# Performance work log

Measured on AMD Instinct MI355X. Metric: run time of the kernel, lower is better.

The kernel has to match this reference:

```python
import jax, jax.numpy as jnp
import numpy as np


def setup_inputs() -> dict:
    key = jax.random.key(0)
    ks = jax.random.split(key, 12)
    Tq, Tk, B, H = 1024, 1024, 8, 1024
    inp = {
        "inputs_q": jax.random.normal(ks[0], (Tq, B, H), jnp.float32),
        "inputs_kv": jax.random.normal(ks[1], (Tk, B, H), jnp.float32),
        "w_q": jax.random.normal(ks[2], (H, H), jnp.float32) * 0.02,
        "b_q": jnp.zeros((H,), jnp.float32),
        "w_kv": jax.random.normal(ks[3], (2 * H, H), jnp.float32) * 0.02,
        "b_kv": jnp.zeros((2 * H,), jnp.float32),
        "w_o": jax.random.normal(ks[4], (H, H), jnp.float32) * 0.02,
        "b_o": jnp.zeros((H,), jnp.float32),
        # BatchEnsemble rank-1 factors, initialized near 1
        "r_q": 1.0 + 0.05 * jax.random.normal(ks[5], (B, H), jnp.float32),
        "s_q": 1.0 + 0.05 * jax.random.normal(ks[6], (B, H), jnp.float32),
        "r_kv": 1.0 + 0.05 * jax.random.normal(ks[7], (B, H), jnp.float32),
        "s_kv": 1.0 + 0.05 * jax.random.normal(ks[8], (B, 2 * H), jnp.float32),
        "heads": 16,
    }
    return inp


def be_linear(x, w, b, r, s):
    # x: [T,B,Hin], w: [Hout,Hin], r: [B,Hin], s: [B,Hout]
    return jnp.einsum('tbh,oh->tbo', x * r, w) * s + b


def reference(inputs_q, inputs_kv, w_q, b_q, w_kv, b_kv, w_o, b_o,
              r_q, s_q, r_kv, s_kv, heads):
    Tq, B, H = inputs_q.shape
    Tk = inputs_kv.shape[0]
    hd = H // heads
    scale = hd ** -0.5

    q = be_linear(inputs_q, w_q, b_q, r_q, s_q)          # [Tq,B,H]
    kv = be_linear(inputs_kv, w_kv, b_kv, r_kv, s_kv)    # [Tk,B,2H]

    queries = q.reshape(Tq, B * heads, hd)
    kv = kv.reshape(Tk, B * heads, 2, hd)                # layout: head x {k,v} x hd
    keys = kv[:, :, 0, :]
    values = kv[:, :, 1, :]

    scores = jnp.einsum('qnd,knd->nqk', queries, keys) * scale  # [B*heads,Tq,Tk]
    probs = jax.nn.softmax(scores.astype(jnp.float32), axis=-1).astype(scores.dtype)
    # dropout_prob = 0 / eval: dropout is identity
    ctx = jnp.einsum('nqk,knd->qnd', probs, values).reshape(Tq, B, H)
    out = jnp.einsum('tbh,oh->tbo', ctx, w_o) + b_o      # [Tq,B,H]
    return out
```

## Files before the change

kernel.cpp:

```cpp
#include <hip/hip_runtime.h>
#include <stdint.h>

typedef unsigned short u16;
typedef __bf16 bf16x8 __attribute__((ext_vector_type(8)));
typedef float f32x4 __attribute__((ext_vector_type(4)));

typedef __attribute__((address_space(3))) void lds_void;
typedef const __attribute__((address_space(1))) void gbl_void;
#define GLD_LDS16(g, l) __builtin_amdgcn_global_load_lds((gbl_void*)(g), (lds_void*)(l), 16, 0, 0)

#define BAR_RELAX() asm volatile("s_waitcnt vmcnt(4)\n\ts_barrier" ::: "memory")
#define BAR_FULL()  asm volatile("s_waitcnt vmcnt(0)\n\ts_barrier" ::: "memory")

__device__ __forceinline__ u16 f2bf(float f) {
  unsigned u = __float_as_uint(f);
  u += 0x7fffu + ((u >> 16) & 1u);
  return (u16)(u >> 16);
}

__device__ __forceinline__ unsigned pk2bf(float a, float b) {
  unsigned au = __float_as_uint(a) + 0x8000u;
  unsigned bu = __float_as_uint(b) + 0x8000u;
  return __builtin_amdgcn_perm(bu, au, 0x07060302u);
}

__global__ void k_convert_all(const float* __restrict__ inq, const float* __restrict__ r_q,
                              const float* __restrict__ inkv, const float* __restrict__ r_kv,
                              const float* __restrict__ w_q, const float* __restrict__ w_kv,
                              const float* __restrict__ w_o,
                              u16* __restrict__ Xq, u16* __restrict__ Xkv,
                              u16* __restrict__ Wq, u16* __restrict__ Wkv,
                              u16* __restrict__ Wo) {
  int blk = blockIdx.x;
  const float* src; const float* r = nullptr; u16* dst; int base;
  if (blk < 8192)       { src = inq;  r = r_q;  dst = Xq;  base = 0; }
  else if (blk < 16384) { src = inkv; r = r_kv; dst = Xkv; base = 8192; }
  else if (blk < 17408) { src = w_q;  dst = Wq;  base = 16384; }
  else if (blk < 19456) { src = w_kv; dst = Wkv; base = 17408; }
  else                  { src = w_o;  dst = Wo;  base = 19456; }
  int i4 = ((blk - base) * 256 + threadIdx.x) * 4;
  float4 xv = *(const float4*)(src + i4);
  if (r) {
    int rb = ((i4 >> 10) & 7) * 1024 + (i4 & 1023);
    float4 rv = *(const float4*)(r + rb);
    xv.x *= rv.x; xv.y *= rv.y; xv.z *= rv.z; xv.w *= rv.w;
  }
  unsigned long long pk = (unsigned long long)pk2bf(xv.x, xv.y)
      | ((unsigned long long)pk2bf(xv.z, xv.w) << 32);
  *(unsigned long long*)(dst + i4) = pk;
}

template <int MODE>
__device__ __forceinline__ void gemm_tile(const u16* __restrict__ A, const u16* __restrict__ B,
                                          void* __restrict__ Cout, const float* __restrict__ s,
                                          const float* __restrict__ bias, int N, int K,
                                          float postscale, int bx, int by,
                                          u16* As, u16* Bs, int tid,
                                          u16* __restrict__ vt, int h) {
  const int w = tid >> 6, lane = tid & 63;
  const int quad = lane >> 4, l16 = lane & 15;
  const int n0 = bx * 128, m0 = by * 128;
  const int wm = (w & 1) * 64, wn = (w >> 1) * 64;

  f32x4 acc[4][4] = {};

  int srow[2], scol[2];
#pragma unroll
  for (int i = 0; i < 2; ++i) {
    int p = (w * 2 + i) * 64 + lane;
    int row = p >> 2;
    int cb = (p & 3) ^ ((row >> 1) & 3);
    srow[i] = row; scol[i] = cb * 8;
  }
  int offA[4], offB[4];
#pragma unroll
  for (int t = 0; t < 4; ++t) {
    int ra = wm + t * 16 + l16;
    offA[t] = ra * 32 + ((quad ^ ((ra >> 1) & 3)) * 8);
    int rb = wn + t * 16 + l16;
    offB[t] = rb * 32 + ((quad ^ ((rb >> 1) & 3)) * 8);
  }

#pragma unroll
  for (int st = 0; st < 2; ++st)
#pragma unroll
    for (int i = 0; i < 2; ++i) {
      GLD_LDS16(A + (size_t)(m0 + srow[i]) * K + st * 32 + scol[i],
                As + st * 4096 + (w * 2 + i) * 512);
      GLD_LDS16(B + (size_t)(n0 + srow[i]) * K + st * 32 + scol[i],
                Bs + st * 4096 + (w * 2 + i) * 512);
    }

  int cur = 0, nxt = 2;
#pragma unroll 1
  for (int k0 = 0; k0 < K; k0 += 32) {
    if (k0 + 32 >= K) BAR_FULL(); else BAR_RELAX();

    if (k0 + 64 < K) {
#pragma unroll
      for (int i = 0; i < 2; ++i) {
        GLD_LDS16(A + (size_t)(m0 + srow[i]) * K + (k0 + 64) + scol[i],
                  As + nxt * 4096 + (w * 2 + i) * 512);
        GLD_LDS16(B + (size_t)(n0 + srow[i]) * K + (k0 + 64) + scol[i],
                  Bs + nxt * 4096 + (w * 2 + i) * 512);
      }
    }
    const u16* Ac = As + cur * 4096;
    const u16* Bc = Bs + cur * 4096;
    bf16x8 af[4], bfr[4];
#pragma unroll
    for (int mt = 0; mt < 4; ++mt) af[mt] = *(const bf16x8*)(Ac + offA[mt]);
#pragma unroll
    for (int nt = 0; nt < 4; ++nt) bfr[nt] = *(const bf16x8*)(Bc + offB[nt]);
#pragma unroll
    for (int mt = 0; mt < 4; ++mt)
#pragma unroll
      for (int nt = 0; nt < 4; ++nt)
        acc[mt][nt] = __builtin_amdgcn_mfma_f32_16x16x32_bf16(bfr[nt], af[mt], acc[mt][nt], 0, 0, 0);
    cur = (cur == 2) ? 0 : cur + 1;
    nxt = (nxt == 2) ? 0 : nxt + 1;
  }

  if (MODE == 0) {
#pragma unroll
    for (int mt = 0; mt < 4; ++mt) {
      const int m = m0 + wm + mt * 16 + l16;
      const size_t rowb = (size_t)m * N;
      const float* srw = s + (m & 7) * N;
#pragma unroll
      for (int nt = 0; nt < 4; ++nt) {
        const int nb = n0 + wn + nt * 16 + quad * 4;
        float4 sv = *(const float4*)(srw + nb);
        float4 bv = *(const float4*)(bias + nb);
        f32x4 a = acc[mt][nt];
        unsigned long long pk =
            (unsigned long long)pk2bf((a[0] * sv.x + bv.x) * postscale,
                                      (a[1] * sv.y + bv.y) * postscale)
          | ((unsigned long long)pk2bf((a[2] * sv.z + bv.z) * postscale,
                                       (a[3] * sv.w + bv.w) * postscale) << 32);
        *(unsigned long long*)((u16*)Cout + rowb + nb) = pk;
      }
    }
  } else if (MODE == 1) {
#pragma unroll
    for (int mt = 0; mt < 4; ++mt) {
      const int m = m0 + wm + mt * 16 + l16;
      const size_t rowb = (size_t)m * N;
#pragma unroll
      for (int nt = 0; nt < 4; ++nt) {
        const int nb = n0 + wn + nt * 16 + quad * 4;
        float4 bv = *(const float4*)(bias + nb);
        f32x4 a = acc[mt][nt];
        float4 o = {a[0] + bv.x, a[1] + bv.y, a[2] + bv.z, a[3] + bv.w};
        *(float4*)((float*)Cout + rowb + nb) = o;
      }
    }
  } else {
    __syncthreads();
    if (wn == 0) {
#pragma unroll
      for (int mt = 0; mt < 4; ++mt) {
        const int m = m0 + wm + mt * 16 + l16;
        const int b = m & 7, tk = m >> 3;
        u16* krow = (u16*)Cout + ((size_t)(tk * 128 + b * 16 + h)) * 64;
        const float* srw = s + (m & 7) * N;
#pragma unroll
        for (int nt = 0; nt < 4; ++nt) {
          const int nb = n0 + nt * 16 + quad * 4;
          float4 sv = *(const float4*)(srw + nb);
          float4 bv = *(const float4*)(bias + nb);
          f32x4 a = acc[mt][nt];
          unsigned long long pk =
              (unsigned long long)pk2bf(a[0] * sv.x + bv.x, a[1] * sv.y + bv.y)
            | ((unsigned long long)pk2bf(a[2] * sv.z + bv.z, a[3] * sv.w + bv.w) << 32);
          *(unsigned long long*)(krow + nt * 16 + quad * 4) = pk;
        }
      }
    } else {
      u16* L = As + (w - 2) * 4608;
#pragma unroll
      for (int mt = 0; mt < 4; ++mt) {
        const int m = m0 + wm + mt * 16 + l16;
        const int b = m & 7;
        const int tkl = (mt * 16 + l16) >> 3;
        const float* srw = s + (m & 7) * N;
#pragma unroll
        for (int nt = 0; nt < 4; ++nt) {
          const int nb = n0 + 64 + nt * 16 + quad * 4;
          float4 sv = *(const float4*)(srw + nb);
          float4 bv = *(const float4*)(bias + nb);
          f32x4 a = acc[mt][nt];
          const int dl = nt * 16 + quad * 4;
          L[(dl + 0) * 72 + b * 8 + tkl] = f2bf(a[0] * sv.x + bv.x);
          L[(dl + 1) * 72 + b * 8 + tkl] = f2bf(a[1] * sv.y + bv.y);
          L[(dl + 2) * 72 + b * 8 + tkl] = f2bf(a[2] * sv.z + bv.z);
          L[(dl + 3) * 72 + b * 8 + tkl] = f2bf(a[3] * sv.w + bv.w);
        }
      }
      asm volatile("s_waitcnt lgkmcnt(0)" ::: "memory");
      const int tk0 = by * 16 + (wm >> 3);
#pragma unroll
      for (int it = 0; it < 8; ++it) {
        const int dloc = it * 8 + (lane >> 3);
        const int b = lane & 7;
        bf16x8 vchunk = *(const bf16x8*)(L + dloc * 72 + b * 8);
        *(bf16x8*)(vt + ((size_t)((b * 16 + h) * 64 + dloc)) * 1024 + tk0) = vchunk;
      }
    }
  }
}

__global__ void k_gemm_qkv(const u16* __restrict__ Xq, const u16* __restrict__ Wq,
                           u16* __restrict__ qout, const float* __restrict__ s_q,
                           const float* __restrict__ b_q, float qscale,
                           const u16* __restrict__ Xkv, const u16* __restrict__ Wkv,
                           u16* __restrict__ kbuf, const float* __restrict__ s_kv,
                           const float* __restrict__ b_kv, u16* __restrict__ vt) {
  __shared__ __align__(16) u16 As[3 * 4096];
  __shared__ __align__(16) u16 Bs[3 * 4096];
  const int blk = blockIdx.x;
  const int xcd = blk & 7;
  const int slot = blk >> 3;
  const int bx = slot % 24;
  const int by = xcd * 8 + slot / 24;
  if (bx < 8)
    gemm_tile<0>(Xq, Wq, qout, s_q, b_q, 1024, 1024, qscale, bx, by, As, Bs,
                 threadIdx.x, nullptr, 0);
  else
    gemm_tile<2>(Xkv, Wkv, kbuf, s_kv, b_kv, 2048, 1024, 1.0f, bx - 8, by, As, Bs,
                 threadIdx.x, vt, bx - 8);
}

__global__ void k_gemm_o(const u16* __restrict__ A, const u16* __restrict__ B,
                         float* __restrict__ Cout, const float* __restrict__ bias) {
  __shared__ __align__(16) u16 As[3 * 4096];
  __shared__ __align__(16) u16 Bs[3 * 4096];
  const int blk = blockIdx.x;
  const int xcd = blk & 7;
  const int slot = blk >> 3;
  const int bx = slot % 8;
  const int by = xcd * 8 + slot / 8;
  gemm_tile<1>(A, B, Cout, nullptr, bias, 1024, 1024, 1.0f, bx, by, As, Bs,
               threadIdx.x, nullptr, 0);
}

__global__ __launch_bounds__(256, 3) void k_attn(const u16* __restrict__ qb,
                                                 const u16* __restrict__ kb,
                                                 const u16* __restrict__ vtb,
                                                 u16* __restrict__ ctx) {
  __shared__ __align__(16) u16 Ks[2][4096];
  __shared__ __align__(16) u16 Vts[2][4096];
  __shared__ __align__(16) u16 Ps[4][32 * 72];

  const int tid = threadIdx.x;
  const int w = tid >> 6, lane = tid & 63;
  const int quad = lane >> 4, l16 = lane & 15;
  const int n = blockIdx.x & 127;
  const int q0 = (blockIdx.x >> 7) << 7;
  const int qw = q0 + w * 32;

  bf16x8 bq[2][2];
#pragma unroll
  for (int g = 0; g < 2; ++g)
#pragma unroll
    for (int ks = 0; ks < 2; ++ks)
      bq[g][ks] = *(const bf16x8*)(qb + ((size_t)(qw + g * 16 + l16) * 128 + n) * 64 + ks * 32 + quad * 8);

  const bool isK = (w < 2);
  const int wv = w & 1;
  const u16* gbase[4];
  u16* lbase[4];
#pragma unroll
  for (int i = 0; i < 4; ++i) {
    int p = (wv * 4 + i) * 64 + lane;
    int r = p >> 3;
    int scb = ((p & 7) ^ (r & 7)) * 8;
    if (isK) {
      gbase[i] = kb + ((size_t)r * 128 + n) * 64 + scb;
      lbase[i] = &Ks[0][(wv * 4 + i) * 512];
    } else {
      gbase[i] = vtb + ((size_t)n * 64 + r) * 1024 + scb;
      lbase[i] = &Vts[0][(wv * 4 + i) * 512];
    }
  }
  const size_t gstep = isK ? 8192 : 1;
  const int lstep = 4096;

  float l_i[2] = {0.f, 0.f};
  f32x4 accO[2][4] = {};
  u16* myP = Ps[w];

#pragma unroll
  for (int i = 0; i < 4; ++i) GLD_LDS16(gbase[i], lbase[i]);

#pragma unroll 1
  for (int tk0 = 0; tk0 < 1024; tk0 += 64) {
    const int cur = (tk0 >> 6) & 1;
    __syncthreads();
    if (tk0 < 960) {
      size_t goff = (size_t)(tk0 + 64) * gstep;
#pragma unroll
      for (int i = 0; i < 4; ++i)
        GLD_LDS16(gbase[i] + goff, lbase[i] + (cur ^ 1) * lstep);
    }
    const u16* Kc = Ks[cur];
    const u16* Vc = Vts[cur];

    f32x4 accS[2][4] = {};
#pragma unroll
    for (int mt = 0; mt < 4; ++mt) {
      int r = mt * 16 + l16;
#pragma unroll
      for (int ks = 0; ks < 2; ++ks) {
        bf16x8 ak = *(const bf16x8*)(Kc + r * 64 + (((ks * 4 + quad) ^ (r & 7)) << 3));
#pragma unroll
        for (int g = 0; g < 2; ++g)
          accS[g][mt] = __builtin_amdgcn_mfma_f32_16x16x32_bf16(ak, bq[g][ks], accS[g][mt], 0, 0, 0);
      }
    }

#pragma unroll
    for (int g = 0; g < 2; ++g) {
      float pv[16];
      float ss = 0.f;
#pragma unroll
      for (int mt = 0; mt < 4; ++mt)
#pragma unroll
        for (int rg = 0; rg < 4; ++rg) {
          float p = __builtin_amdgcn_exp2f(accS[g][mt][rg]);
          pv[mt * 4 + rg] = p;
          ss += p;
        }
      ss += __shfl_xor(ss, 16);
      ss += __shfl_xor(ss, 32);
      l_i[g] += ss;
      const int prow = (g * 16 + l16) * 72;
#pragma unroll
      for (int mt = 0; mt < 4; ++mt) {
        unsigned long long pk = (unsigned long long)pk2bf(pv[mt * 4 + 0], pv[mt * 4 + 1])
            | ((unsigned long long)pk2bf(pv[mt * 4 + 2], pv[mt * 4 + 3]) << 32);
        *(unsigned long long*)(myP + prow + mt * 16 + quad * 4) = pk;
      }
    }

    bf16x8 bp[2][2];
#pragma unroll
    for (int g = 0; g < 2; ++g)
#pragma unroll
      for (int ks = 0; ks < 2; ++ks)
        bp[g][ks] = *(const bf16x8*)(myP + (g * 16 + l16) * 72 + ks * 32 + quad * 8);
#pragma unroll
    for (int dt = 0; dt < 4; ++dt) {
      int r = dt * 16 + l16;
#pragma unroll
      for (int ks = 0; ks < 2; ++ks) {
        bf16x8 av = *(const bf16x8*)(Vc + r * 64 + (((ks * 4 + quad) ^ (r & 7)) << 3));
#pragma unroll
        for (int g = 0; g < 2; ++g)
          accO[g][dt] = __builtin_amdgcn_mfma_f32_16x16x32_bf16(av, bp[g][ks], accO[g][dt], 0, 0, 0);
      }
    }
  }

#pragma unroll
  for (int g = 0; g < 2; ++g) {
    float inv = 1.f / l_i[g];
    const size_t obase = ((size_t)(qw + g * 16 + l16) * 128 + n) * 64;
#pragma unroll
    for (int dt = 0; dt < 4; ++dt) {
      unsigned long long pk = (unsigned long long)pk2bf(accO[g][dt][0] * inv, accO[g][dt][1] * inv)
          | ((unsigned long long)pk2bf(accO[g][dt][2] * inv, accO[g][dt][3] * inv) << 32);
      *(unsigned long long*)(ctx + obase + dt * 16 + quad * 4) = pk;
    }
  }
}

extern "C" void kernel_launch(void* const* d_in, const int* in_sizes, int n_in,
                              void* d_out, int out_size, void* d_ws, size_t ws_size,
                              hipStream_t stream) {
  const float* inq  = (const float*)d_in[0];
  const float* inkv = (const float*)d_in[1];
  const float* w_q  = (const float*)d_in[2];
  const float* b_q  = (const float*)d_in[3];
  const float* w_kv = (const float*)d_in[4];
  const float* b_kv = (const float*)d_in[5];
  const float* w_o  = (const float*)d_in[6];
  const float* b_o  = (const float*)d_in[7];
  const float* r_q  = (const float*)d_in[8];
  const float* s_q  = (const float*)d_in[9];
  const float* r_kv = (const float*)d_in[10];
  const float* s_kv = (const float*)d_in[11];

  const size_t MEG = 1024 * 1024;
  u16* ws    = (u16*)d_ws;
  u16* Xq    = ws;
  u16* Xkv   = ws + 8 * MEG;
  u16* Wq    = ws + 16 * MEG;
  u16* Wkv   = ws + 17 * MEG;
  u16* Wo    = ws + 19 * MEG;
  u16* qbuf  = ws + 20 * MEG;
  u16* kbuf  = ws + 28 * MEG;
  u16* vt    = ws + 36 * MEG;
  u16* ctx   = Xq;

  k_convert_all<<<20480, 256, 0, stream>>>(inq, r_q, inkv, r_kv, w_q, w_kv, w_o,
                                           Xq, Xkv, Wq, Wkv, Wo);

  const float QSCALE = 0.125f * 1.44269504088896340736f;
  k_gemm_qkv<<<1536, 256, 0, stream>>>(Xq, Wq, qbuf, s_q, b_q, QSCALE,
                                       Xkv, Wkv, kbuf, s_kv, b_kv, vt);
  k_attn<<<1024, 256, 0, stream>>>(qbuf, kbuf, vt, ctx);
  k_gemm_o<<<512, 256, 0, stream>>>(ctx, Wo, (float*)d_out, b_o);
}
```

Before: 286.9 us.

## Read K and V tiles directly from global memory in attention kernel

Removes the double-buffered LDS staging of K and V tiles, along with the async global-to-LDS loads and the per-iteration barrier. Each wave now loads its MFMA operands straight from global memory and relies on the L1/L2 caches for reuse across the four waves. This drops the synchronisation and LDS traffic but gives up explicit prefetch overlap, and each K/V tile is now fetched by every wave rather than once per block.

```diff
diff --git a/kernel.cpp b/kernel.cpp
--- a/kernel.cpp
+++ b/kernel.cpp
@@ -248,8 +248,6 @@
                                                  const u16* __restrict__ kb,
                                                  const u16* __restrict__ vtb,
                                                  u16* __restrict__ ctx) {
-  __shared__ __align__(16) u16 Ks[2][4096];
-  __shared__ __align__(16) u16 Vts[2][4096];
   __shared__ __align__(16) u16 Ps[4][32 * 72];
 
   const int tid = threadIdx.x;
@@ -266,53 +264,22 @@
     for (int ks = 0; ks < 2; ++ks)
       bq[g][ks] = *(const bf16x8*)(qb + ((size_t)(qw + g * 16 + l16) * 128 + n) * 64 + ks * 32 + quad * 8);
 
-  const bool isK = (w < 2);
-  const int wv = w & 1;
-  const u16* gbase[4];
-  u16* lbase[4];
-#pragma unroll
-  for (int i = 0; i < 4; ++i) {
-    int p = (wv * 4 + i) * 64 + lane;
-    int r = p >> 3;
-    int scb = ((p & 7) ^ (r & 7)) * 8;
-    if (isK) {
-      gbase[i] = kb + ((size_t)r * 128 + n) * 64 + scb;
-      lbase[i] = &Ks[0][(wv * 4 + i) * 512];
-    } else {
-      gbase[i] = vtb + ((size_t)n * 64 + r) * 1024 + scb;
-      lbase[i] = &Vts[0][(wv * 4 + i) * 512];
-    }
-  }
-  const size_t gstep = isK ? 8192 : 1;
-  const int lstep = 4096;
+  const u16* kbase = kb + (size_t)n * 64;
+  const u16* vbase = vtb + ((size_t)n << 16);
 
   float l_i[2] = {0.f, 0.f};
   f32x4 accO[2][4] = {};
   u16* myP = Ps[w];
 
-#pragma unroll
-  for (int i = 0; i < 4; ++i) GLD_LDS16(gbase[i], lbase[i]);
-
 #pragma unroll 1
   for (int tk0 = 0; tk0 < 1024; tk0 += 64) {
-    const int cur = (tk0 >> 6) & 1;
-    __syncthreads();
-    if (tk0 < 960) {
-      size_t goff = (size_t)(tk0 + 64) * gstep;
-#pragma unroll
-      for (int i = 0; i < 4; ++i)
-        GLD_LDS16(gbase[i] + goff, lbase[i] + (cur ^ 1) * lstep);
-    }
-    const u16* Kc = Ks[cur];
-    const u16* Vc = Vts[cur];
-
     f32x4 accS[2][4] = {};
 #pragma unroll
     for (int mt = 0; mt < 4; ++mt) {
-      int r = mt * 16 + l16;
+      const size_t rb = (size_t)(tk0 + mt * 16 + l16) * 8192;
 #pragma unroll
       for (int ks = 0; ks < 2; ++ks) {
-        bf16x8 ak = *(const bf16x8*)(Kc + r * 64 + (((ks * 4 + quad) ^ (r & 7)) << 3));
+        bf16x8 ak = *(const bf16x8*)(kbase + rb + ks * 32 + quad * 8);
 #pragma unroll
         for (int g = 0; g < 2; ++g)
           accS[g][mt] = __builtin_amdgcn_mfma_f32_16x16x32_bf16(ak, bq[g][ks], accS[g][mt], 0, 0, 0);
@@ -349,12 +316,13 @@
 #pragma unroll
       for (int ks = 0; ks < 2; ++ks)
         bp[g][ks] = *(const bf16x8*)(myP + (g * 16 + l16) * 72 + ks * 32 + quad * 8);
+
 #pragma unroll
     for (int dt = 0; dt < 4; ++dt) {
-      int r = dt * 16 + l16;
+      const size_t rb = (size_t)(dt * 16 + l16) * 1024 + tk0;
 #pragma unroll
       for (int ks = 0; ks < 2; ++ks) {
-        bf16x8 av = *(const bf16x8*)(Vc + r * 64 + (((ks * 4 + quad) ^ (r & 7)) << 3));
+        bf16x8 av = *(const bf16x8*)(vbase + rb + ks * 32 + quad * 8);
 #pragma unroll
         for (int g = 0; g < 2; ++g)
           accO[g][dt] = __builtin_amdgcn_mfma_f32_16x16x32_bf16(av, bp[g][ks], accO[g][dt], 0, 0, 0);
```

Measured after the change: 355.0 us. 23.8% more time.
